# Optimization experiments

Measured on AMD Instinct MI355X. Metric: run time of the kernel, lower is better.

## Reference

```python
import jax, jax.numpy as jnp
import numpy as np

N_WORD, N_DOC, E = 20000, 20000, 500000
H, O, D = 4, 32, 128  # heads, out per head, hidden*heads
NEG_SLOPE = 0.2


def setup_inputs() -> dict:
    key = jax.random.key(0)
    ks = jax.random.split(key, 24)
    rn = lambda k, s, sc=0.1: jax.random.normal(k, s, dtype=jnp.float32) * sc
    ri = lambda k, s, hi: jax.random.randint(k, s, 0, hi, dtype=jnp.int32)
    return {
        'x_word': rn(ks[0], (N_WORD, 300), 1.0),
        'x_doc': rn(ks[1], (N_DOC, D), 1.0),
        'Wp_word': rn(ks[2], (300, D)), 'bp_word': jnp.zeros((D,), jnp.float32),
        'Wp_doc': rn(ks[3], (D, D)), 'bp_doc': jnp.zeros((D,), jnp.float32),
        'Wsrc': rn(ks[4], (2, 3, D, D)), 'bsrc': jnp.zeros((2, 3, D), jnp.float32),
        'Wdst': rn(ks[5], (2, 3, D, D)), 'bdst': jnp.zeros((2, 3, D), jnp.float32),
        'attn': rn(ks[6], (2, 3, H, O)), 'bconv': jnp.zeros((2, 3, D), jnp.float32),
        'Wc1': rn(ks[7], (D, 64)), 'bc1': jnp.zeros((64,), jnp.float32),
        'Wc2': rn(ks[8], (64, 64)), 'bc2': jnp.zeros((64,), jnp.float32),
        'src_wd': ri(ks[9], (E,), N_WORD), 'dst_wd': ri(ks[10], (E,), N_DOC),
        'src_dw': ri(ks[11], (E,), N_DOC), 'dst_dw': ri(ks[12], (E,), N_WORD),
        'src_dd': ri(ks[13], (E,), N_DOC), 'dst_dd': ri(ks[14], (E,), N_DOC),
    }


def _gatv2(h_src, h_dst, src, dst, Ws, bs, Wd, bd, a, bias, n_dst):
    # GATv2Conv (DGL): e = a . leaky_relu(Ws h_u + Wd h_v); edge softmax per dst; sum alpha*Ws h_u
    fs = (h_src @ Ws + bs).reshape(-1, H, O)           # [N_src,H,O]
    fd = (h_dst @ Wd + bd).reshape(-1, H, O)           # [N_dst,H,O]
    e = jax.nn.leaky_relu(fs[src] + fd[dst], NEG_SLOPE)  # [E,H,O]
    score = jnp.einsum('eho,ho->eh', e, a)             # [E,H]
    m = jax.lax.stop_gradient(jax.ops.segment_max(score, dst, num_segments=n_dst))
    ex = jnp.exp(score - m[dst])
    s = jax.ops.segment_sum(ex, dst, num_segments=n_dst)
    alpha = ex / s[dst]                                 # per-dst softmax
    rst = jax.ops.segment_sum(alpha[:, :, None] * fs[src], dst, num_segments=n_dst)
    return rst + bias.reshape(1, H, O)


def reference(x_word, x_doc, Wp_word, bp_word, Wp_doc, bp_doc, Wsrc, bsrc, Wdst, bdst,
              attn, bconv, Wc1, bc1, Wc2, bc2, src_wd, dst_wd, src_dw, dst_dw, src_dd, dst_dd):
    h_w = x_word @ Wp_word + bp_word
    h_d = x_doc @ Wp_doc + bp_doc
    for l in range(2):
        o_wd = _gatv2(h_w, h_d, src_wd, dst_wd, Wsrc[l, 0], bsrc[l, 0], Wdst[l, 0], bdst[l, 0], attn[l, 0], bconv[l, 0], N_DOC)
        o_dw = _gatv2(h_d, h_w, src_dw, dst_dw, Wsrc[l, 1], bsrc[l, 1], Wdst[l, 1], bdst[l, 1], attn[l, 1], bconv[l, 1], N_WORD)
        o_dd = _gatv2(h_d, h_d, src_dd, dst_dd, Wsrc[l, 2], bsrc[l, 2], Wdst[l, 2], bdst[l, 2], attn[l, 2], bconv[l, 2], N_DOC)
        h_d = ((o_wd + o_dd) * 0.5).reshape(N_DOC, D)   # mean over 2 relations into 'document'
        h_w = o_dw.reshape(N_WORD, D)                    # mean over 1 relation into 'word'
    z = jax.nn.relu(h_d @ Wc1 + bc1)
    return z @ Wc2 + bc2  # [N_DOC, len_label]
```

## Files before the change

kernel.cpp:

```cpp
#include <hip/hip_runtime.h>

#define NNODE 20000
#define NEDGE 500000
#define CAP 64
#define RCHUNK 2048
#define NRANGE 8
#define RSZ 2500
#define SCAP 70000
#define XW 64

typedef __attribute__((ext_vector_type(8))) short bf16x8;
typedef __attribute__((ext_vector_type(8))) unsigned short u16x8;
typedef __attribute__((ext_vector_type(4))) float f32x4;

__device__ __forceinline__ unsigned short f2bf(float f) {
    unsigned u = __float_as_uint(f);
    return (unsigned short)((u + 0x7FFFu + ((u >> 16) & 1u)) >> 16);
}
__device__ __forceinline__ float bf2f(unsigned short h) {
    return __uint_as_float((unsigned)h << 16);
}

__device__ __forceinline__ void split_one(
    const float* __restrict__ B, unsigned short* __restrict__ Bt,
    int K, int N, int Kp, int i)
{
    int n = i / Kp, k = i % Kp;
    float v = (k < K) ? B[(size_t)k * N + n] : 0.f;
    unsigned short h = f2bf(v);
    Bt[i] = h;
    Bt[(size_t)N * Kp + i] = f2bf(v - bf2f(h));
}

__device__ __forceinline__ void split_row4(
    const float* __restrict__ X, unsigned short* __restrict__ A2,
    int K, int Kp, int r, int c)
{
    float v[4];
#pragma unroll
    for (int j = 0; j < 4; ++j) v[j] = (c + j < K) ? X[(size_t)r * K + c + j] : 0.f;
    ushort4 hi, lo;
    unsigned short h;
    h = f2bf(v[0]); hi.x = h; lo.x = f2bf(v[0] - bf2f(h));
    h = f2bf(v[1]); hi.y = h; lo.y = f2bf(v[1] - bf2f(h));
    h = f2bf(v[2]); hi.z = h; lo.z = f2bf(v[2] - bf2f(h));
    h = f2bf(v[3]); hi.w = h; lo.w = f2bf(v[3] - bf2f(h));
    *reinterpret_cast<ushort4*>(A2 + (size_t)r * 2 * Kp + c) = hi;
    *reinterpret_cast<ushort4*>(A2 + (size_t)r * 2 * Kp + Kp + c) = lo;
}

#define RB_ROUTE ((NEDGE + RCHUNK - 1) / RCHUNK)

__global__ __launch_bounds__(256) void build_prep_kernel(
    const int* __restrict__ s0, const int* __restrict__ d0,
    const int* __restrict__ s1, const int* __restrict__ d1,
    const int* __restrict__ s2, const int* __restrict__ d2,
    unsigned* __restrict__ stage, int* __restrict__ scur,
    const float* __restrict__ Wp_word, const float* __restrict__ Wp_doc,
    const float* __restrict__ Wsrc, const float* __restrict__ Wdst,
    const float* __restrict__ Wc1, const float* __restrict__ Wc2,
    const float* __restrict__ xw, const float* __restrict__ xd,
    unsigned short* __restrict__ WtPw, unsigned short* __restrict__ WtPd,
    unsigned short* __restrict__ WtCat,
    unsigned short* __restrict__ WtC1, unsigned short* __restrict__ WtC2,
    unsigned short* __restrict__ Ax, unsigned short* __restrict__ Axd)
{
    __shared__ unsigned sbuf[RCHUNK];
    __shared__ int hcnt[NRANGE], hoff[NRANGE], gbase[NRANGE], hcur[NRANGE];
    const int tid = threadIdx.x;
    if ((int)blockIdx.x < 3 * RB_ROUTE) {
        const int rel = blockIdx.x / RB_ROUTE;
        const int c0 = (blockIdx.x % RB_ROUTE) * RCHUNK;
        const int n = (c0 + RCHUNK <= NEDGE) ? RCHUNK : (NEDGE - c0);
        const int* sp = rel == 0 ? s0 : rel == 1 ? s1 : s2;
        const int* dp = rel == 0 ? d0 : rel == 1 ? d1 : d2;

        if (tid < NRANGE) hcnt[tid] = 0;
        __syncthreads();
        for (int i = tid; i < n; i += 256) atomicAdd(&hcnt[dp[c0 + i] / RSZ], 1);
        __syncthreads();
        if (tid == 0) {
            int o = 0;
            for (int r = 0; r < NRANGE; ++r) {
                hoff[r] = o; hcur[r] = o; o += hcnt[r];
                gbase[r] = atomicAdd(&scur[rel * NRANGE + r], hcnt[r]);
            }
        }
        __syncthreads();
        for (int i = tid; i < n; i += 256) {
            int d = dp[c0 + i], s = sp[c0 + i];
            int k = atomicAdd(&hcur[d / RSZ], 1);
            sbuf[k] = ((unsigned)d << 16) | (unsigned)s;
        }
        __syncthreads();
        for (int r = 0; r < NRANGE; ++r) {
            int cnt = hcnt[r];
            int lim = SCAP - gbase[r];
            if (cnt > lim) cnt = lim;
            unsigned* dst = stage + (size_t)(rel * NRANGE + r) * SCAP + gbase[r];
            for (int i = tid; i < cnt; i += 256) dst[i] = sbuf[hoff[r] + i];
        }
        return;
    }
    int i = ((int)blockIdx.x - 3 * RB_ROUTE) * 256 + tid;
    const int S0 = 128 * 320, S1 = 128 * 128, S2 = 6 * 256 * 128;
    const int S3 = 64 * 128, S4 = 64 * 64;
    const int X1 = NNODE * 80, X2 = NNODE * 32;
    if (i < S0) { split_one(Wp_word, WtPw, 300, 128, 320, i); return; }
    i -= S0;
    if (i < S1) { split_one(Wp_doc, WtPd, 128, 128, 128, i); return; }
    i -= S1;
    if (i < S2) {
        int lc = i / (256 * 128), rem = i % (256 * 128);
        int n = rem / 128, k = rem % 128;
        int l = lc / 3, c = lc % 3;
        int half = n >> 7, nn = n & 127;
        const float* M;
        if (c == 0)      M = half ? (Wdst + (size_t)(l * 3 + 1) * 16384) : (Wsrc + (size_t)(l * 3 + 0) * 16384);
        else if (c == 1) M = half ? (Wsrc + (size_t)(l * 3 + 1) * 16384) : (Wdst + (size_t)(l * 3 + 0) * 16384);
        else             M = half ? (Wdst + (size_t)(l * 3 + 2) * 16384) : (Wsrc + (size_t)(l * 3 + 2) * 16384);
        float v = M[(size_t)k * 128 + nn];
        unsigned short h = f2bf(v);
        unsigned short* Bt = WtCat + (size_t)lc * 65536;
        Bt[(size_t)n * 128 + k] = h;
        Bt[32768 + (size_t)n * 128 + k] = f2bf(v - bf2f(h));
        return;
    }
    i -= S2;
    if (i < S3) { split_one(Wc1, WtC1, 128, 64, 128, i); return; }
    i -= S3;
    if (i < S4) { split_one(Wc2, WtC2, 64, 64, 64, i); return; }
    i -= S4;
    if (i < X1) {
        int r = i / 80, c = (i % 80) * 4;
        split_row4(xw, Ax, 300, 320, r, c);
        return;
    }
    i -= X1;
    if (i < X2) {
        int r = i / 32, c = (i % 32) * 4;
        split_row4(xd, Axd, 128, 128, r, c);
    }
}

__global__ __launch_bounds__(256) void xfill_kernel(
    const unsigned* __restrict__ stage, const int* __restrict__ scur,
    int* __restrict__ deg, unsigned short* __restrict__ csr)
{
    const int r = blockIdx.x & 7;
    const int w = blockIdx.x >> 3;
    const int tid = threadIdx.x;
#pragma unroll
    for (int rel = 0; rel < 3; ++rel) {
        int total = scur[rel * NRANGE + r];
        if (total > SCAP) total = SCAP;
        const unsigned* st = stage + (size_t)(rel * NRANGE + r) * SCAP;
        int* dg = deg + rel * NNODE;
        unsigned short* cb = csr + (size_t)rel * NNODE * CAP;
        for (int i = w * 256 + tid; i < total; i += XW * 256) {
            unsigned p = st[i];
            int d = (int)(p >> 16), s = (int)(p & 0xFFFFu);
            int k = atomicAdd(&dg[d], 1);
            if (k < CAP) cb[(size_t)d * CAP + k] = (unsigned short)s;
        }
    }
}

template<int BM, int BN, int MODE>
__device__ __forceinline__ void gemm_body(
    const unsigned short* __restrict__ A2,
    const unsigned short* __restrict__ Bt,
    const float* __restrict__ b0,
    float* __restrict__ C0, unsigned short* __restrict__ S0,
    int M, int Kp, int do_relu, int m0,
    unsigned short (*As)[BM][40], unsigned short (*Bs)[BN][40])
{
    constexpr int FM = BM / 32;
    constexpr int FN = BN / 64;
    const int tid = threadIdx.x;
    const int wid = tid >> 6, lane = tid & 63;
    const int wm = wid >> 2, wn = wid & 3;
    const int lr = lane & 15, kg = lane >> 4;

    f32x4 acc[FM][FN] = {};
    const size_t KA = 2 * (size_t)Kp;
    const size_t PB = (size_t)BN * Kp;

    for (int k0 = 0; k0 < Kp; k0 += 32) {
#pragma unroll
        for (int idx = tid; idx < BM * 4; idx += 512) {
            int row = idx >> 2, ck = idx & 3;
            u16x8 hi = {0,0,0,0,0,0,0,0}, lo = {0,0,0,0,0,0,0,0};
            if (m0 + row < M) {
                const unsigned short* ap = A2 + (size_t)(m0 + row) * KA + k0 + ck * 8;
                hi = *reinterpret_cast<const u16x8*>(ap);
                lo = *reinterpret_cast<const u16x8*>(ap + Kp);
            }
            *reinterpret_cast<u16x8*>(&As[0][row][ck * 8]) = hi;
            *reinterpret_cast<u16x8*>(&As[1][row][ck * 8]) = lo;
        }
#pragma unroll
        for (int idx = tid; idx < BN * 4; idx += 512) {
            int nr = idx >> 2, ck = idx & 3;
            const unsigned short* bp = Bt + (size_t)nr * Kp + k0 + ck * 8;
            *reinterpret_cast<u16x8*>(&Bs[0][nr][ck * 8]) = *reinterpret_cast<const u16x8*>(bp);
            *reinterpret_cast<u16x8*>(&Bs[1][nr][ck * 8]) = *reinterpret_cast<const u16x8*>(bp + PB);
        }
        __syncthreads();
        bf16x8 ah[FM], al[FM], bh[FN], bl[FN];
#pragma unroll
        for (int fm = 0; fm < FM; ++fm) {
            ah[fm] = *reinterpret_cast<const bf16x8*>(&As[0][wm * (BM / 2) + fm * 16 + lr][kg * 8]);
            al[fm] = *reinterpret_cast<const bf16x8*>(&As[1][wm * (BM / 2) + fm * 16 + lr][kg * 8]);
        }
#pragma unroll
        for (int fn = 0; fn < FN; ++fn) {
            bh[fn] = *reinterpret_cast<const bf16x8*>(&Bs[0][wn * (BN / 4) + fn * 16 + lr][kg * 8]);
            bl[fn] = *reinterpret_cast<const bf16x8*>(&Bs[1][wn * (BN / 4) + fn * 16 + lr][kg * 8]);
        }
#pragma unroll
        for (int fm = 0; fm < FM; ++fm)
#pragma unroll
            for (int fn = 0; fn < FN; ++fn) {
                acc[fm][fn] = __builtin_amdgcn_mfma_f32_16x16x32_bf16(ah[fm], bh[fn], acc[fm][fn], 0, 0, 0);
                acc[fm][fn] = __builtin_amdgcn_mfma_f32_16x16x32_bf16(al[fm], bh[fn], acc[fm][fn], 0, 0, 0);
                acc[fm][fn] = __builtin_amdgcn_mfma_f32_16x16x32_bf16(ah[fm], bl[fn], acc[fm][fn], 0, 0, 0);
            }
        __syncthreads();
    }
#pragma unroll
    for (int fm = 0; fm < FM; ++fm)
#pragma unroll
        for (int fn = 0; fn < FN; ++fn) {
            int gc = wn * (BN / 4) + fn * 16 + lr;
            float bv = b0[gc];
#pragma unroll
            for (int j = 0; j < 4; ++j) {
                int gr = m0 + wm * (BM / 2) + fm * 16 + kg * 4 + j;
                if (gr < M) {
                    float v = acc[fm][fn][j] + bv;
                    if (do_relu) v = fmaxf(v, 0.f);
                    if (MODE == 0) {
                        C0[(size_t)gr * BN + gc] = v;
                    } else {
                        unsigned short h = f2bf(v);
                        S0[(size_t)gr * 2 * BN + gc] = h;
                        S0[(size_t)gr * 2 * BN + BN + gc] = f2bf(v - bf2f(h));
                    }
                }
            }
        }
}

template<int BM, int BN, int MODE>
__global__ __launch_bounds__(512) void gemm_mfma_kernel(
    const unsigned short* __restrict__ A2,
    const unsigned short* __restrict__ Bt,
    const float* __restrict__ b0,
    float* __restrict__ C0, unsigned short* __restrict__ S0,
    int M, int Kp, int do_relu)
{
    __shared__ unsigned short As[2][BM][40];
    __shared__ unsigned short Bs[2][BN][40];
    gemm_body<BM, BN, MODE>(A2, Bt, b0, C0, S0, M, Kp, do_relu,
                            blockIdx.x * BM, As, Bs);
}

struct Proj2Args {
    const unsigned short* A[2];
    const unsigned short* Bt[2];
    const float* b0[2];
    unsigned short* S0[2];
    int Kp[2];
};

__global__ __launch_bounds__(512) void gemm_proj2_kernel(Proj2Args a, int M)
{
    __shared__ unsigned short As[2][128][40];
    __shared__ unsigned short Bs[2][128][40];
    const int y = blockIdx.y;
    gemm_body<128, 128, 2>(a.A[y], a.Bt[y], a.b0[y], nullptr, a.S0[y],
                           M, a.Kp[y], 0, blockIdx.x * 128, As, Bs);
}

struct Cat3Args {
    const unsigned short* A[3];
    const unsigned short* Bt[3];
    const float* bs0[3];
    const float* bs1[3];
    unsigned short* P0[3];
    unsigned short* P1[3];
};

__global__ __launch_bounds__(512) void gemm_cat3_kernel(Cat3Args args, int M)
{
    constexpr int BM = 128, BN = 256, FM = 4, FN = 4, Kp = 128;
    const int y = blockIdx.y;
    const unsigned short* __restrict__ A2 = args.A[y];
    const unsigned short* __restrict__ Bt = args.Bt[y];
    __shared__ unsigned short As[2][BM][40];
    __shared__ unsigned short Bs[2][BN][40];
    const int tid = threadIdx.x;
    const int m0 = blockIdx.x * BM;
    const int wid = tid >> 6, lane = tid & 63;
    const int wm = wid >> 2, wn = wid & 3;
    const int lr = lane & 15, kg = lane >> 4;

    f32x4 acc[FM][FN] = {};
    const size_t KA = 2 * (size_t)Kp;
    const size_t PB = (size_t)BN * Kp;

    for (int k0 = 0; k0 < Kp; k0 += 32) {
#pragma unroll
        for (int idx = tid; idx < BM * 4; idx += 512) {
            int row = idx >> 2, ck = idx & 3;
            u16x8 hi = {0,0,0,0,0,0,0,0}, lo = {0,0,0,0,0,0,0,0};
            if (m0 + row < M) {
                const unsigned short* ap = A2 + (size_t)(m0 + row) * KA + k0 + ck * 8;
                hi = *reinterpret_cast<const u16x8*>(ap);
                lo = *reinterpret_cast<const u16x8*>(ap + Kp);
            }
            *reinterpret_cast<u16x8*>(&As[0][row][ck * 8]) = hi;
            *reinterpret_cast<u16x8*>(&As[1][row][ck * 8]) = lo;
        }
#pragma unroll
        for (int idx = tid; idx < BN * 4; idx += 512) {
            int nr = idx >> 2, ck = idx & 3;
            const unsigned short* bp = Bt + (size_t)nr * Kp + k0 + ck * 8;
            *reinterpret_cast<u16x8*>(&Bs[0][nr][ck * 8]) = *reinterpret_cast<const u16x8*>(bp);
            *reinterpret_cast<u16x8*>(&Bs[1][nr][ck * 8]) = *reinterpret_cast<const u16x8*>(bp + PB);
        }
        __syncthreads();
        bf16x8 ah[FM], al[FM], bh[FN], bl[FN];
#pragma unroll
        for (int fm = 0; fm < FM; ++fm) {
            ah[fm] = *reinterpret_cast<const bf16x8*>(&As[0][wm * 64 + fm * 16 + lr][kg * 8]);
            al[fm] = *reinterpret_cast<const bf16x8*>(&As[1][wm * 64 + fm * 16 + lr][kg * 8]);
        }
#pragma unroll
        for (int fn = 0; fn < FN; ++fn) {
            bh[fn] = *reinterpret_cast<const bf16x8*>(&Bs[0][wn * 64 + fn * 16 + lr][kg * 8]);
            bl[fn] = *reinterpret_cast<const bf16x8*>(&Bs[1][wn * 64 + fn * 16 + lr][kg * 8]);
        }
#pragma unroll
        for (int fm = 0; fm < FM; ++fm)
#pragma unroll
            for (int fn = 0; fn < FN; ++fn) {
                acc[fm][fn] = __builtin_amdgcn_mfma_f32_16x16x32_bf16(ah[fm], bh[fn], acc[fm][fn], 0, 0, 0);
                acc[fm][fn] = __builtin_amdgcn_mfma_f32_16x16x32_bf16(al[fm], bh[fn], acc[fm][fn], 0, 0, 0);
                acc[fm][fn] = __builtin_amdgcn_mfma_f32_16x16x32_bf16(ah[fm], bl[fn], acc[fm][fn], 0, 0, 0);
            }
        __syncthreads();
    }
    const float* __restrict__ bs0 = args.bs0[y];
    const float* __restrict__ bs1 = args.bs1[y];
    unsigned short* __restrict__ P0 = args.P0[y];
    unsigned short* __restrict__ P1 = args.P1[y];
#pragma unroll
    for (int fm = 0; fm < FM; ++fm)
#pragma unroll
        for (int fn = 0; fn < FN; ++fn) {
            int gc = wn * 64 + fn * 16 + lr;
            float bv = (gc < 128) ? bs0[gc] : bs1[gc - 128];
#pragma unroll
            for (int j = 0; j < 4; ++j) {
                int gr = m0 + wm * 64 + fm * 16 + kg * 4 + j;
                if (gr < M) {
                    float v = acc[fm][fn][j] + bv;
                    unsigned short h = f2bf(v);
                    if (gc < 128) P0[(size_t)gr * 128 + gc] = h;
                    else          P1[(size_t)gr * 128 + gc - 128] = h;
                }
            }
        }
}

__device__ __forceinline__ void rel_raw(
    const unsigned short* __restrict__ fsP,
    const unsigned short* __restrict__ fdP,
    const unsigned short* __restrict__ csrc,
    const float* __restrict__ attnRow,
    int d, int lane, int iBeg, int iEnd,
    float& ssum, float* __restrict__ acc)
{
    float fdv[8], av[8];
    {
        u16x8 t = *reinterpret_cast<const u16x8*>(fdP + (size_t)d * 128 + lane * 8);
#pragma unroll
        for (int j = 0; j < 8; ++j) fdv[j] = bf2f(t[j]);
    }
#pragma unroll
    for (int j = 0; j < 8; ++j) av[j] = attnRow[lane * 8 + j];

    int i = iBeg;
    for (; i + 4 <= iEnd; i += 4) {
        int s0 = csrc[i], s1 = csrc[i + 1], s2 = csrc[i + 2], s3 = csrc[i + 3];
        u16x8 q0 = *reinterpret_cast<const u16x8*>(fsP + (size_t)s0 * 128 + lane * 8);
        u16x8 q1 = *reinterpret_cast<const u16x8*>(fsP + (size_t)s1 * 128 + lane * 8);
        u16x8 q2 = *reinterpret_cast<const u16x8*>(fsP + (size_t)s2 * 128 + lane * 8);
        u16x8 q3 = *reinterpret_cast<const u16x8*>(fsP + (size_t)s3 * 128 + lane * 8);
        float u0[8], u1[8], u2[8], u3[8];
        float pa0 = 0.f, pb0 = 0.f, pa1 = 0.f, pb1 = 0.f;
        float pa2 = 0.f, pb2 = 0.f, pa3 = 0.f, pb3 = 0.f;
#pragma unroll
        for (int j = 0; j < 8; ++j) {
            u0[j] = bf2f(q0[j]); float z = u0[j] + fdv[j];
            pa0 = fmaf(av[j], z, pa0); pb0 = fmaf(av[j], fabsf(z), pb0);
        }
#pragma unroll
        for (int j = 0; j < 8; ++j) {
            u1[j] = bf2f(q1[j]); float z = u1[j] + fdv[j];
            pa1 = fmaf(av[j], z, pa1); pb1 = fmaf(av[j], fabsf(z), pb1);
        }
#pragma unroll
        for (int j = 0; j < 8; ++j) {
            u2[j] = bf2f(q2[j]); float z = u2[j] + fdv[j];
            pa2 = fmaf(av[j], z, pa2); pb2 = fmaf(av[j], fabsf(z), pb2);
        }
#pragma unroll
        for (int j = 0; j < 8; ++j) {
            u3[j] = bf2f(q3[j]); float z = u3[j] + fdv[j];
            pa3 = fmaf(av[j], z, pa3); pb3 = fmaf(av[j], fabsf(z), pb3);
        }
        float p0 = fmaf(0.4f, pb0, 0.6f * pa0);
        float p1 = fmaf(0.4f, pb1, 0.6f * pa1);
        float p2 = fmaf(0.4f, pb2, 0.6f * pa2);
        float p3 = fmaf(0.4f, pb3, 0.6f * pa3);
        p0 += __shfl_xor(p0, 1); p0 += __shfl_xor(p0, 2);
        p1 += __shfl_xor(p1, 1); p1 += __shfl_xor(p1, 2);
        p2 += __shfl_xor(p2, 1); p2 += __shfl_xor(p2, 2);
        p3 += __shfl_xor(p3, 1); p3 += __shfl_xor(p3, 2);
        float w0 = __expf(p0), w1 = __expf(p1);
        float w2 = __expf(p2), w3 = __expf(p3);
        ssum += (w0 + w1) + (w2 + w3);
#pragma unroll
        for (int j = 0; j < 8; ++j)
            acc[j] += fmaf(w0, u0[j], w1 * u1[j]) + fmaf(w2, u2[j], w3 * u3[j]);
    }
    for (; i < iEnd; ++i) {
        int s0 = csrc[i];
        u16x8 q0 = *reinterpret_cast<const u16x8*>(fsP + (size_t)s0 * 128 + lane * 8);
        float u0[8];
        float pa = 0.f, pb = 0.f;
#pragma unroll
        for (int j = 0; j < 8; ++j) {
            u0[j] = bf2f(q0[j]); float z = u0[j] + fdv[j];
            pa = fmaf(av[j], z, pa); pb = fmaf(av[j], fabsf(z), pb);
        }
        float p0 = fmaf(0.4f, pb, 0.6f * pa);
        p0 += __shfl_xor(p0, 1); p0 += __shfl_xor(p0, 2);
        float w = __expf(p0);
        ssum += w;
#pragma unroll
        for (int j = 0; j < 8; ++j) acc[j] = fmaf(w, u0[j], acc[j]);
    }
}

struct ConvJob {
    const unsigned short *fsA, *fdA;
    const int* degA; const unsigned short* csrA;
    const float *attnA, *biasA;
    const unsigned short *fsB, *fdB;
    const int* degB; const unsigned short* csrB;
    const float *attnB, *biasB;
    float wscale;
    unsigned short* sp;
};

__global__ __launch_bounds__(256) void gat_conv4_kernel(
    ConvJob J0, ConvJob J1, int nblk0)
{
    const bool first = ((int)blockIdx.x < nblk0);
    const ConvJob J = first ? J0 : J1;
    const int b = first ? (int)blockIdx.x : (int)blockIdx.x - nblk0;
    const int tid = threadIdx.x;
    const int d = b * 4 + (tid >> 6);
    const int lane = tid & 15;
    const int group = (tid >> 4) & 3;
    if (d >= NNODE) return;

    float ssum = 0.f;
    float acc[8];
#pragma unroll
    for (int j = 0; j < 8; ++j) acc[j] = 0.f;
    float r[8];

    if (J.fsB) {
        const int rel = group >> 1, hf = group & 1;
        const unsigned short* fs = rel ? J.fsB : J.fsA;
        const unsigned short* fd = rel ? J.fdB : J.fdA;
        const int* dgp           = rel ? J.degB : J.degA;
        const unsigned short* cs = rel ? J.csrB : J.csrA;
        const float* at          = rel ? J.attnB : J.attnA;
        int deg = dgp[d]; if (deg > CAP) deg = CAP;
        int h0 = (deg + 1) >> 1;
        int iB = d * CAP + (hf ? h0 : 0);
        int iE = d * CAP + (hf ? deg : h0);
        rel_raw(fs, fd, cs, at, d, lane, iB, iE, ssum, acc);
        ssum += __shfl_xor(ssum, 16);
#pragma unroll
        for (int j = 0; j < 8; ++j) acc[j] += __shfl_xor(acc[j], 16);
        float inv = (ssum > 0.f) ? J.wscale / ssum : 0.f;
#pragma unroll
        for (int j = 0; j < 8; ++j) {
            r[j] = inv * acc[j];
            r[j] += __shfl_xor(r[j], 32);
        }
    } else {
        int deg = J.degA[d]; if (deg > CAP) deg = CAP;
        int iB = d * CAP + ((deg * group) >> 2);
        int iE = d * CAP + ((deg * (group + 1)) >> 2);
        rel_raw(J.fsA, J.fdA, J.csrA, J.attnA, d, lane, iB, iE, ssum, acc);
        ssum += __shfl_xor(ssum, 16);
        ssum += __shfl_xor(ssum, 32);
#pragma unroll
        for (int j = 0; j < 8; ++j) {
            acc[j] += __shfl_xor(acc[j], 16);
            acc[j] += __shfl_xor(acc[j], 32);
        }
        float inv = (ssum > 0.f) ? J.wscale / ssum : 0.f;
#pragma unroll
        for (int j = 0; j < 8; ++j) r[j] = inv * acc[j];
    }

    if (group == 0) {
        u16x8 hv, lv;
#pragma unroll
        for (int j = 0; j < 8; ++j) {
            float bb = J.biasA[lane * 8 + j];
            if (J.biasB) bb += J.biasB[lane * 8 + j];
            float o = J.wscale * bb + r[j];
            unsigned short hh = f2bf(o);
            hv[j] = hh;
            lv[j] = f2bf(o - bf2f(hh));
        }
        *reinterpret_cast<u16x8*>(J.sp + (size_t)d * 256 + lane * 8) = hv;
        *reinterpret_cast<u16x8*>(J.sp + (size_t)d * 256 + 128 + lane * 8) = lv;
    }
}

extern "C" void kernel_launch(void* const* d_in, const int* in_sizes, int n_in,
                              void* d_out, int out_size, void* d_ws, size_t ws_size,
                              hipStream_t stream)
{
    const float* x_word  = (const float*)d_in[0];
    const float* x_doc   = (const float*)d_in[1];
    const float* Wp_word = (const float*)d_in[2];
    const float* bp_word = (const float*)d_in[3];
    const float* Wp_doc  = (const float*)d_in[4];
    const float* bp_doc  = (const float*)d_in[5];
    const float* Wsrc    = (const float*)d_in[6];
    const float* bsrc    = (const float*)d_in[7];
    const float* Wdst    = (const float*)d_in[8];
    const float* bdst    = (const float*)d_in[9];
    const float* attn    = (const float*)d_in[10];
    const float* bconv   = (const float*)d_in[11];
    const float* Wc1     = (const float*)d_in[12];
    const float* bc1     = (const float*)d_in[13];
    const float* Wc2     = (const float*)d_in[14];
    const float* bc2     = (const float*)d_in[15];
    const int* src_wd = (const int*)d_in[16];
    const int* dst_wd = (const int*)d_in[17];
    const int* src_dw = (const int*)d_in[18];
    const int* dst_dw = (const int*)d_in[19];
    const int* src_dd = (const int*)d_in[20];
    const int* dst_dd = (const int*)d_in[21];

    const size_t NP = (size_t)NNODE * 128;
    unsigned short* U = (unsigned short*)d_ws;
    unsigned short* Pfs_wd = U;
    unsigned short* Pfd_dw = U + 1 * NP;
    unsigned short* Pfd_wd = U + 2 * NP;
    unsigned short* Pfs_dw = U + 3 * NP;
    unsigned short* Pfs_dd = U + 4 * NP;
    unsigned short* Pfd_dd = U + 5 * NP;
    unsigned short* AswA = U + 6 * NP;
    unsigned short* AsdA = AswA + 2 * NP;
    unsigned short* AswB = AsdA + 2 * NP;
    unsigned short* AsdB = AswB + 2 * NP;
    unsigned short* WtPw  = AsdB + 2 * NP;
    unsigned short* WtPd  = WtPw + 81920;
    unsigned short* WtCat = WtPd + 32768;
    unsigned short* WtC1  = WtCat + 393216;
    unsigned short* WtC2  = WtC1 + 16384;
    unsigned short* Ax  = Pfs_wd;
    unsigned short* Axd = AswB;
    unsigned short* Az  = AswB;
    int* I    = (int*)(WtC2 + 8192);
    int* deg  = I;
    int* scur = I + 3 * NNODE;
    unsigned* stage = (unsigned*)(scur + 32);
    unsigned short* csrp = (unsigned short*)(stage + 3 * NRANGE * SCAP);

    const int GB128 = (NNODE + 127) / 128;
    const int CB4 = (NNODE + 3) / 4;
    const int PREP = 266240 + NNODE * 112;
    const int BPB = 3 * RB_ROUTE + (PREP + 255) / 256;

    (void)hipMemsetAsync(deg, 0, (3 * NNODE + 32) * sizeof(int), stream);
    build_prep_kernel<<<BPB, 256, 0, stream>>>(
        src_wd, dst_wd, src_dw, dst_dw, src_dd, dst_dd, stage, scur,
        Wp_word, Wp_doc, Wsrc, Wdst, Wc1, Wc2, x_word, x_doc,
        WtPw, WtPd, WtCat, WtC1, WtC2, Ax, Axd);
    xfill_kernel<<<NRANGE * XW, 256, 0, stream>>>(stage, scur, deg, csrp);

    Proj2Args pa;
    pa.A[0] = Ax;  pa.Bt[0] = WtPw; pa.b0[0] = bp_word; pa.S0[0] = AswA; pa.Kp[0] = 320;
    pa.A[1] = Axd; pa.Bt[1] = WtPd; pa.b0[1] = bp_doc;  pa.S0[1] = AsdA; pa.Kp[1] = 128;
    gemm_proj2_kernel<<<dim3(GB128, 2), 512, 0, stream>>>(pa, NNODE);

    const unsigned short* Asw_in = AswA;
    const unsigned short* Asd_in = AsdA;
    for (int l = 0; l < 2; ++l) {
        const int l3 = l * 3;
        Cat3Args ca;
        ca.A[0] = Asw_in; ca.A[1] = Asd_in; ca.A[2] = Asd_in;
        ca.Bt[0] = WtCat + (size_t)(l3 + 0) * 65536;
        ca.Bt[1] = WtCat + (size_t)(l3 + 1) * 65536;
        ca.Bt[2] = WtCat + (size_t)(l3 + 2) * 65536;
        ca.bs0[0] = bsrc + (l3 + 0) * 128; ca.bs1[0] = bdst + (l3 + 1) * 128;
        ca.bs0[1] = bdst + (l3 + 0) * 128; ca.bs1[1] = bsrc + (l3 + 1) * 128;
        ca.bs0[2] = bsrc + (l3 + 2) * 128; ca.bs1[2] = bdst + (l3 + 2) * 128;
        ca.P0[0] = Pfs_wd; ca.P1[0] = Pfd_dw;
        ca.P0[1] = Pfd_wd; ca.P1[1] = Pfs_dw;
        ca.P0[2] = Pfs_dd; ca.P1[2] = Pfd_dd;
        gemm_cat3_kernel<<<dim3(GB128, 3), 512, 0, stream>>>(ca, NNODE);

        ConvJob jd;
        jd.fsA = Pfs_wd; jd.fdA = Pfd_wd; jd.degA = deg;             jd.csrA = csrp;
        jd.attnA = attn + (l3 + 0) * 128; jd.biasA = bconv + (l3 + 0) * 128;
        jd.fsB = Pfs_dd; jd.fdB = Pfd_dd; jd.degB = deg + 2 * NNODE; jd.csrB = csrp + (size_t)2 * NNODE * CAP;
        jd.attnB = attn + (l3 + 2) * 128; jd.biasB = bconv + (l3 + 2) * 128;
        jd.wscale = 0.5f; jd.sp = (l == 0 ? AsdB : AsdA);

        if (l == 0) {
            ConvJob jw;
            jw.fsA = Pfs_dw; jw.fdA = Pfd_dw; jw.degA = deg + NNODE; jw.csrA = csrp + (size_t)NNODE * CAP;
            jw.attnA = attn + (l3 + 1) * 128; jw.biasA = bconv + (l3 + 1) * 128;
            jw.fsB = nullptr; jw.fdB = nullptr; jw.degB = nullptr; jw.csrB = nullptr;
            jw.attnB = nullptr; jw.biasB = nullptr;
            jw.wscale = 1.0f; jw.sp = AswB;
            gat_conv4_kernel<<<2 * CB4, 256, 0, stream>>>(jd, jw, CB4);
        } else {
            gat_conv4_kernel<<<CB4, 256, 0, stream>>>(jd, jd, CB4);
        }
        Asw_in = AswB;
        Asd_in = AsdB;
    }

    gemm_mfma_kernel<128, 64, 2><<<GB128, 512, 0, stream>>>(
        AsdA, WtC1, bc1, nullptr, Az, NNODE, 128, 1);
    gemm_mfma_kernel<128, 64, 0><<<GB128, 512, 0, stream>>>(
        Az, WtC2, bc2, (float*)d_out, nullptr, NNODE, 64, 0);
}
```

Measured before the change: 369.5 us.

## Assign 32 lanes per destination node and unroll edge gather by eight

Each GAT conv destination node is now handled by 32 threads instead of 64. In the doc kernel each relation gets one 16-lane half that walks all of that relation's edges. In the word kernel the edge list is split into two halves. The edge loop gains an 8-way unrolled path that issues eight row gathers at once, to expose more memory-level parallelism, and the 4-way path is reordered. This halves the threads per node and lengthens each thread's serial edge walk, and the wider unroll raises register pressure in exchange for more loads in flight.

```diff
diff --git a/kernel.cpp b/kernel.cpp
--- a/kernel.cpp
+++ b/kernel.cpp
@@ -393,39 +393,70 @@
     for (int j = 0; j < 8; ++j) av[j] = attnRow[lane * 8 + j];
 
     int i = iBeg;
+    for (; i + 8 <= iEnd; i += 8) {
+        int s[8];
+#pragma unroll
+        for (int k = 0; k < 8; ++k) s[k] = csrc[i + k];
+        u16x8 q[8];
+#pragma unroll
+        for (int k = 0; k < 8; ++k)
+            q[k] = *reinterpret_cast<const u16x8*>(fsP + (size_t)s[k] * 128 + lane * 8);
+        float p[8];
+#pragma unroll
+        for (int k = 0; k < 8; ++k) {
+            float pa = 0.f, pb = 0.f;
+#pragma unroll
+            for (int j = 0; j < 8; ++j) {
+                float z = bf2f(q[k][j]) + fdv[j];
+                pa = fmaf(av[j], z, pa);
+                pb = fmaf(av[j], fabsf(z), pb);
+            }
+            p[k] = fmaf(0.4f, pb, 0.6f * pa);
+        }
+#pragma unroll
+        for (int k = 0; k < 8; ++k) {
+            p[k] += __shfl_xor(p[k], 1);
+            p[k] += __shfl_xor(p[k], 2);
+        }
+        float w[8];
+#pragma unroll
+        for (int k = 0; k < 8; ++k) w[k] = __expf(p[k]);
+        ssum += ((w[0] + w[1]) + (w[2] + w[3])) + ((w[4] + w[5]) + (w[6] + w[7]));
+#pragma unroll
+        for (int j = 0; j < 8; ++j) {
+            float t0 = fmaf(w[0], bf2f(q[0][j]), w[1] * bf2f(q[1][j]));
+            float t1 = fmaf(w[2], bf2f(q[2][j]), w[3] * bf2f(q[3][j]));
+            float t2 = fmaf(w[4], bf2f(q[4][j]), w[5] * bf2f(q[5][j]));
+            float t3 = fmaf(w[6], bf2f(q[6][j]), w[7] * bf2f(q[7][j]));
+            acc[j] += (t0 + t1) + (t2 + t3);
+        }
+    }
     for (; i + 4 <= iEnd; i += 4) {
         int s0 = csrc[i], s1 = csrc[i + 1], s2 = csrc[i + 2], s3 = csrc[i + 3];
         u16x8 q0 = *reinterpret_cast<const u16x8*>(fsP + (size_t)s0 * 128 + lane * 8);
         u16x8 q1 = *reinterpret_cast<const u16x8*>(fsP + (size_t)s1 * 128 + lane * 8);
         u16x8 q2 = *reinterpret_cast<const u16x8*>(fsP + (size_t)s2 * 128 + lane * 8);
         u16x8 q3 = *reinterpret_cast<const u16x8*>(fsP + (size_t)s3 * 128 + lane * 8);
-        float u0[8], u1[8], u2[8], u3[8];
-        float pa0 = 0.f, pb0 = 0.f, pa1 = 0.f, pb1 = 0.f;
-        float pa2 = 0.f, pb2 = 0.f, pa3 = 0.f, pb3 = 0.f;
-#pragma unroll
-        for (int j = 0; j < 8; ++j) {
-            u0[j] = bf2f(q0[j]); float z = u0[j] + fdv[j];
-            pa0 = fmaf(av[j], z, pa0); pb0 = fmaf(av[j], fabsf(z), pb0);
-        }
-#pragma unroll
-        for (int j = 0; j < 8; ++j) {
-            u1[j] = bf2f(q1[j]); float z = u1[j] + fdv[j];
-            pa1 = fmaf(av[j], z, pa1); pb1 = fmaf(av[j], fabsf(z), pb1);
-        }
-#pragma unroll
-        for (int j = 0; j < 8; ++j) {
-            u2[j] = bf2f(q2[j]); float z = u2[j] + fdv[j];
-            pa2 = fmaf(av[j], z, pa2); pb2 = fmaf(av[j], fabsf(z), pb2);
-        }
-#pragma unroll
-        for (int j = 0; j < 8; ++j) {
-            u3[j] = bf2f(q3[j]); float z = u3[j] + fdv[j];
-            pa3 = fmaf(av[j], z, pa3); pb3 = fmaf(av[j], fabsf(z), pb3);
-        }
-        float p0 = fmaf(0.4f, pb0, 0.6f * pa0);
-        float p1 = fmaf(0.4f, pb1, 0.6f * pa1);
-        float p2 = fmaf(0.4f, pb2, 0.6f * pa2);
-        float p3 = fmaf(0.4f, pb3, 0.6f * pa3);
+        float p0 = 0.f, p1 = 0.f, p2 = 0.f, p3 = 0.f;
+        {
+            float pa0 = 0.f, pb0 = 0.f, pa1 = 0.f, pb1 = 0.f;
+            float pa2 = 0.f, pb2 = 0.f, pa3 = 0.f, pb3 = 0.f;
+#pragma unroll
+            for (int j = 0; j < 8; ++j) {
+                float z0 = bf2f(q0[j]) + fdv[j];
+                float z1 = bf2f(q1[j]) + fdv[j];
+                float z2 = bf2f(q2[j]) + fdv[j];
+                float z3 = bf2f(q3[j]) + fdv[j];
+                pa0 = fmaf(av[j], z0, pa0); pb0 = fmaf(av[j], fabsf(z0), pb0);
+                pa1 = fmaf(av[j], z1, pa1); pb1 = fmaf(av[j], fabsf(z1), pb1);
+                pa2 = fmaf(av[j], z2, pa2); pb2 = fmaf(av[j], fabsf(z2), pb2);
+                pa3 = fmaf(av[j], z3, pa3); pb3 = fmaf(av[j], fabsf(z3), pb3);
+            }
+            p0 = fmaf(0.4f, pb0, 0.6f * pa0);
+            p1 = fmaf(0.4f, pb1, 0.6f * pa1);
+            p2 = fmaf(0.4f, pb2, 0.6f * pa2);
+            p3 = fmaf(0.4f, pb3, 0.6f * pa3);
+        }
         p0 += __shfl_xor(p0, 1); p0 += __shfl_xor(p0, 2);
         p1 += __shfl_xor(p1, 1); p1 += __shfl_xor(p1, 2);
         p2 += __shfl_xor(p2, 1); p2 += __shfl_xor(p2, 2);
@@ -435,16 +466,16 @@
         ssum += (w0 + w1) + (w2 + w3);
 #pragma unroll
         for (int j = 0; j < 8; ++j)
-            acc[j] += fmaf(w0, u0[j], w1 * u1[j]) + fmaf(w2, u2[j], w3 * u3[j]);
+            acc[j] += fmaf(w0, bf2f(q0[j]), w1 * bf2f(q1[j]))
+                    + fmaf(w2, bf2f(q2[j]), w3 * bf2f(q3[j]));
     }
     for (; i < iEnd; ++i) {
         int s0 = csrc[i];
         u16x8 q0 = *reinterpret_cast<const u16x8*>(fsP + (size_t)s0 * 128 + lane * 8);
-        float u0[8];
         float pa = 0.f, pb = 0.f;
 #pragma unroll
         for (int j = 0; j < 8; ++j) {
-            u0[j] = bf2f(q0[j]); float z = u0[j] + fdv[j];
+            float z = bf2f(q0[j]) + fdv[j];
             pa = fmaf(av[j], z, pa); pb = fmaf(av[j], fabsf(z), pb);
         }
         float p0 = fmaf(0.4f, pb, 0.6f * pa);
@@ -452,7 +483,7 @@
         float w = __expf(p0);
         ssum += w;
 #pragma unroll
-        for (int j = 0; j < 8; ++j) acc[j] = fmaf(w, u0[j], acc[j]);
+        for (int j = 0; j < 8; ++j) acc[j] = fmaf(w, bf2f(q0[j]), acc[j]);
     }
 }
 
@@ -467,16 +498,16 @@
     unsigned short* sp;
 };
 
-__global__ __launch_bounds__(256) void gat_conv4_kernel(
+__global__ __launch_bounds__(256) void gat_conv6_kernel(
     ConvJob J0, ConvJob J1, int nblk0)
 {
     const bool first = ((int)blockIdx.x < nblk0);
     const ConvJob J = first ? J0 : J1;
     const int b = first ? (int)blockIdx.x : (int)blockIdx.x - nblk0;
-    const int tid = threadIdx.x;
-    const int d = b * 4 + (tid >> 6);
-    const int lane = tid & 15;
-    const int group = (tid >> 4) & 3;
+    int gid = b * 256 + threadIdx.x;
+    int d = gid >> 5;
+    int lane = gid & 15;
+    int half = (gid >> 4) & 1;
     if (d >= NNODE) return;
 
     float ssum = 0.f;
@@ -486,44 +517,34 @@
     float r[8];
 
     if (J.fsB) {
-        const int rel = group >> 1, hf = group & 1;
-        const unsigned short* fs = rel ? J.fsB : J.fsA;
-        const unsigned short* fd = rel ? J.fdB : J.fdA;
-        const int* dgp           = rel ? J.degB : J.degA;
-        const unsigned short* cs = rel ? J.csrB : J.csrA;
-        const float* at          = rel ? J.attnB : J.attnA;
+        const unsigned short* fs = half ? J.fsB : J.fsA;
+        const unsigned short* fd = half ? J.fdB : J.fdA;
+        const int* dgp           = half ? J.degB : J.degA;
+        const unsigned short* cs = half ? J.csrB : J.csrA;
+        const float* at          = half ? J.attnB : J.attnA;
         int deg = dgp[d]; if (deg > CAP) deg = CAP;
-        int h0 = (deg + 1) >> 1;
-        int iB = d * CAP + (hf ? h0 : 0);
-        int iE = d * CAP + (hf ? deg : h0);
-        rel_raw(fs, fd, cs, at, d, lane, iB, iE, ssum, acc);
+        rel_raw(fs, fd, cs, at, d, lane, d * CAP, d * CAP + deg, ssum, acc);
+        float inv = (ssum > 0.f) ? J.wscale / ssum : 0.f;
+#pragma unroll
+        for (int j = 0; j < 8; ++j) {
+            r[j] = inv * acc[j];
+            r[j] += __shfl_xor(r[j], 16);
+        }
+    } else {
+        int deg = J.degA[d]; if (deg > CAP) deg = CAP;
+        int h = (deg + 1) >> 1;
+        int iB = d * CAP + (half ? h : 0);
+        int iE = d * CAP + (half ? deg : h);
+        rel_raw(J.fsA, J.fdA, J.csrA, J.attnA, d, lane, iB, iE, ssum, acc);
         ssum += __shfl_xor(ssum, 16);
 #pragma unroll
         for (int j = 0; j < 8; ++j) acc[j] += __shfl_xor(acc[j], 16);
         float inv = (ssum > 0.f) ? J.wscale / ssum : 0.f;
 #pragma unroll
-        for (int j = 0; j < 8; ++j) {
-            r[j] = inv * acc[j];
-            r[j] += __shfl_xor(r[j], 32);
-        }
-    } else {
-        int deg = J.degA[d]; if (deg > CAP) deg = CAP;
-        int iB = d * CAP + ((deg * group) >> 2);
-        int iE = d * CAP + ((deg * (group + 1)) >> 2);
-        rel_raw(J.fsA, J.fdA, J.csrA, J.attnA, d, lane, iB, iE, ssum, acc);
-        ssum += __shfl_xor(ssum, 16);
-        ssum += __shfl_xor(ssum, 32);
-#pragma unroll
-        for (int j = 0; j < 8; ++j) {
-            acc[j] += __shfl_xor(acc[j], 16);
-            acc[j] += __shfl_xor(acc[j], 32);
-        }
-        float inv = (ssum > 0.f) ? J.wscale / ssum : 0.f;
-#pragma unroll
         for (int j = 0; j < 8; ++j) r[j] = inv * acc[j];
     }
 
-    if (group == 0) {
+    if (half == 0) {
         u16x8 hv, lv;
 #pragma unroll
         for (int j = 0; j < 8; ++j) {
@@ -593,7 +614,7 @@
     unsigned short* csrp = (unsigned short*)(stage + 3 * NRANGE * SCAP);
 
     const int GB128 = (NNODE + 127) / 128;
-    const int CB4 = (NNODE + 3) / 4;
+    const int CB32 = (NNODE * 32) / 256;
     const int PREP = 266240 + NNODE * 112;
     const int BPB = 3 * RB_ROUTE + (PREP + 255) / 256;
 
@@ -640,9 +661,9 @@
             jw.fsB = nullptr; jw.fdB = nullptr; jw.degB = nullptr; jw.csrB = nullptr;
             jw.attnB = nullptr; jw.biasB = nullptr;
             jw.wscale = 1.0f; jw.sp = AswB;
-            gat_conv4_kernel<<<2 * CB4, 256, 0, stream>>>(jd, jw, CB4);
+            gat_conv6_kernel<<<2 * CB32, 256, 0, stream>>>(jd, jw, CB32);
         } else {
-            gat_conv4_kernel<<<CB4, 256, 0, stream>>>(jd, jd, CB4);
+            gat_conv6_kernel<<<CB32, 256, 0, stream>>>(jd, jd, CB32);
         }
         Asw_in = AswB;
         Asd_in = AsdB;
```

Result: no change. 363.7 us (-1.6%).
